# Kernel tuning notes

Hardware: AMD Instinct MI355X
Metric: run time of the kernel (lower is better)

Reference implementation:

```python
import jax, jax.numpy as jnp
import numpy as np

N = 50000          # nodes
E_RAND = 800000    # random edges
E = E_RAND + N     # + self loops -> 850000
F_IN = 256         # nembed
F_HID = 64         # nhid
H = 8              # nheads
NCLASS = 40
ALPHA = 0.2        # leakyrelu slope


def setup_inputs() -> dict:
    key = jax.random.key(0)
    ks = jax.random.split(key, 8)
    x = jax.random.normal(ks[0], (N, F_IN), dtype=jnp.float32)
    # random edges + self loops (guarantees every row-sum > 0, like adj + I)
    er = jax.random.randint(ks[1], (2, E_RAND), 0, N, dtype=jnp.int32)
    loops = jnp.tile(jnp.arange(N, dtype=jnp.int32)[None, :], (2, 1))
    edge_index = jnp.concatenate([er, loops], axis=1)  # [2, E]
    # per-head attention params (xavier-ish scale)
    W = jax.random.normal(ks[2], (H, F_IN, F_HID), dtype=jnp.float32) * (1.0 / np.sqrt(F_IN))
    a = jax.random.normal(ks[3], (H, 2 * F_HID), dtype=jnp.float32) * 0.1
    Wo = jax.random.normal(ks[4], (H * F_HID, F_HID), dtype=jnp.float32) * (1.0 / np.sqrt(H * F_HID))
    ao = jax.random.normal(ks[5], (2 * F_HID,), dtype=jnp.float32) * 0.1
    mlp_w = jax.random.normal(ks[6], (NCLASS, F_HID), dtype=jnp.float32) * 0.05
    mlp_b = jnp.zeros((NCLASS,), dtype=jnp.float32)
    return {"x": x, "edge_index": edge_index, "W": W, "a": a,
            "Wo": Wo, "ao": ao, "mlp_w": mlp_w, "mlp_b": mlp_b}


def _leaky(v):
    return jnp.where(v > 0, v, ALPHA * v)


def _spgat_layer(x, W, a, src, dst, n):
    """pyGAT SpGraphAttentionLayer (eval mode, dropout = identity).
    out[i] = sum_{e: src=i} exp(-leakyrelu(a.[h_src;h_dst])) * h[dst] / rowsum_i
    """
    h = x @ W                         # [N, D]
    D = W.shape[1]
    s_src = h @ a[:D]                 # [N]
    s_dst = h @ a[D:]                 # [N]
    # per-edge unnormalized attention (note the -exp(leaky) of original sp impl)
    e = jnp.exp(-_leaky(s_src[src] + s_dst[dst]))          # [E]
    rowsum = jax.ops.segment_sum(e, src, num_segments=n)   # [N]
    num = jax.ops.segment_sum(e[:, None] * h[dst], src, num_segments=n)  # [N, D]
    return num / rowsum[:, None]


def reference(x, edge_index, W, a, Wo, ao, mlp_w, mlp_b):
    src, dst = edge_index[0], edge_index[1]
    # multi-head attention, concat=True -> elu inside each head
    heads = [jax.nn.elu(_spgat_layer(x, W[i], a[i], src, dst, N)) for i in range(H)]
    xc = jnp.concatenate(heads, axis=1)                     # [N, H*F_HID]
    # dropout (eval) = identity
    xo = jax.nn.elu(_spgat_layer(xc, Wo, ao, src, dst, N))  # [N, F_HID]
    return xo @ mlp_w.T + mlp_b                             # [N, NCLASS]
```

## Files before the change

kernel.cpp:

```cpp
#include <hip/hip_runtime.h>

#define NN 50000
#define HH 8
#define ALPHA 0.2f
#define NPAD 50048

typedef short short8 __attribute__((ext_vector_type(8)));
typedef float f32x4 __attribute__((ext_vector_type(4)));

__device__ __forceinline__ float elu_f(float x) {
  return x > 0.f ? x : __expf(x) - 1.f;
}

__device__ __forceinline__ unsigned short f2bf(float f) {
  unsigned int u = __float_as_uint(f);
  unsigned int r = (u + 0x7fffu + ((u >> 16) & 1u)) >> 16;
  return (unsigned short)r;
}

__global__ void cvt_w_kernel(const float* __restrict__ W, unsigned short* __restrict__ Wt,
                             const float* __restrict__ Wo, unsigned short* __restrict__ Wot) {
  int tid = blockIdx.x * 256 + threadIdx.x;
  if (tid < HH * 256 * 64) {
    int h = tid / (256 * 64);
    int rem = tid - h * 256 * 64;
    int k = rem >> 6, c = rem & 63;
    Wt[((size_t)h * 64 + c) * 256 + k] = f2bf(W[tid]);
    return;
  }
  int t2 = tid - HH * 256 * 64;
  if (t2 < 512 * 64) {
    int k = t2 >> 6, c = t2 & 63;
    Wot[(size_t)c * 512 + k] = f2bf(Wo[t2]);
  }
}

__global__ void hist_kernel(const int* __restrict__ src, int* __restrict__ cnt, int E) {
  int e = blockIdx.x * blockDim.x + threadIdx.x;
  if (e < E) atomicAdd(&cnt[src[e]], 1);
}

__global__ __launch_bounds__(1024) void scan_blocks_kernel(const int* __restrict__ cnt,
    int* __restrict__ tmp, int* __restrict__ bsum, int n) {
  __shared__ int sh[1024];
  int i = blockIdx.x * 1024 + threadIdx.x;
  int v = (i < n) ? cnt[i] : 0;
  sh[threadIdx.x] = v;
  __syncthreads();
  for (int off = 1; off < 1024; off <<= 1) {
    int t = (threadIdx.x >= off) ? sh[threadIdx.x - off] : 0;
    __syncthreads();
    sh[threadIdx.x] += t;
    __syncthreads();
  }
  if (i < n) tmp[i] = sh[threadIdx.x] - v;
  if (threadIdx.x == 1023) bsum[blockIdx.x] = sh[1023];
}

__global__ __launch_bounds__(64) void scan_top_kernel(const int* __restrict__ bsum,
    int* __restrict__ boffs, int nb) {
  int L = threadIdx.x;
  int v = (L < nb) ? bsum[L] : 0;
  int incl = v;
#pragma unroll
  for (int off = 1; off < 64; off <<= 1) {
    int t = __shfl_up(incl, off, 64);
    if (L >= off) incl += t;
  }
  if (L < nb) boffs[L] = incl - v;
}

__global__ __launch_bounds__(1024) void scan_apply_kernel(const int* __restrict__ tmp,
    const int* __restrict__ boffs, int* __restrict__ row_ptr, int* __restrict__ nxt,
    int n, int E) {
  int i = blockIdx.x * 1024 + threadIdx.x;
  if (i < n) {
    int s = tmp[i] + boffs[blockIdx.x];
    row_ptr[i] = s;
    nxt[i] = s;
  }
  if (i == 0) row_ptr[n] = E;
}

__global__ void scatter_kernel(const int* __restrict__ src, const int* __restrict__ dst,
                               int* __restrict__ nxt, int* __restrict__ col, int E) {
  int e = blockIdx.x * blockDim.x + threadIdx.x;
  if (e < E) {
    int p = atomicAdd(&nxt[src[e]], 1);
    col[p] = dst[e];
  }
}

__global__ __launch_bounds__(256) void mfma_gemm1_kernel(
    const float* __restrict__ X, const unsigned short* __restrict__ Bt,
    const float* __restrict__ Aatt, unsigned short* __restrict__ Cout,
    float* __restrict__ ss, float* __restrict__ sd, int N) {
  __shared__ unsigned short Bs[64][264];
  int w = threadIdx.x >> 6, L = threadIdx.x & 63;
  int quad = L >> 4, l16 = L & 15;
  int m0 = blockIdx.x * 64;
  int myrow = m0 + w * 16 + l16;
  int rowc = min(myrow, N - 1);

  const float* Ar = X + (size_t)rowc * 256 + quad * 8;
  short8 areg[8];
#pragma unroll
  for (int ks = 0; ks < 8; ++ks) {
    float4 a0 = *(const float4*)(Ar + ks * 32);
    float4 a1 = *(const float4*)(Ar + ks * 32 + 4);
    areg[ks][0] = (short)f2bf(a0.x); areg[ks][1] = (short)f2bf(a0.y);
    areg[ks][2] = (short)f2bf(a0.z); areg[ks][3] = (short)f2bf(a0.w);
    areg[ks][4] = (short)f2bf(a1.x); areg[ks][5] = (short)f2bf(a1.y);
    areg[ks][6] = (short)f2bf(a1.z); areg[ks][7] = (short)f2bf(a1.w);
  }

  for (int y = 0; y < HH; ++y) {
    __syncthreads();
    {
      const unsigned short* Bsrc = Bt + (size_t)y * 64 * 256;
      for (int c = threadIdx.x; c < 2048; c += 256) {
        int n = c >> 5;
        int kq = (c & 31) << 3;
        *(uint4*)&Bs[n][kq] = *(const uint4*)(Bsrc + (size_t)n * 256 + kq);
      }
    }
    __syncthreads();

    f32x4 acc[4];
#pragma unroll
    for (int nt = 0; nt < 4; ++nt) acc[nt] = (f32x4)(0.f);
#pragma unroll
    for (int ks = 0; ks < 8; ++ks) {
#pragma unroll
      for (int nt = 0; nt < 4; ++nt) {
        short8 b = *(const short8*)&Bs[l16 + 16 * nt][ks * 32 + quad * 8];
        acc[nt] = __builtin_amdgcn_mfma_f32_16x16x32_bf16(areg[ks], b, acc[nt], 0, 0, 0);
      }
    }

    float as[4], ad[4];
#pragma unroll
    for (int nt = 0; nt < 4; ++nt) {
      as[nt] = Aatt[y * 128 + l16 + 16 * nt];
      ad[nt] = Aatt[y * 128 + 64 + l16 + 16 * nt];
    }
#pragma unroll
    for (int reg = 0; reg < 4; ++reg) {
      float p = 0.f, q = 0.f;
#pragma unroll
      for (int nt = 0; nt < 4; ++nt) {
        p += acc[nt][reg] * as[nt];
        q += acc[nt][reg] * ad[nt];
      }
#pragma unroll
      for (int off = 1; off < 16; off <<= 1) {
        p += __shfl_xor(p, off, 64);
        q += __shfl_xor(q, off, 64);
      }
      int row = m0 + w * 16 + quad * 4 + reg;
      if (l16 == 0 && row < N) {
        ss[(size_t)row * 8 + y] = p;
        sd[(size_t)row * 8 + y] = q;
      }
    }
#pragma unroll
    for (int reg = 0; reg < 4; ++reg) {
      int row = m0 + w * 16 + quad * 4 + reg;
      if (row < N) {
#pragma unroll
        for (int nt = 0; nt < 4; ++nt)
          Cout[(size_t)row * 512 + y * 64 + l16 + 16 * nt] = f2bf(acc[nt][reg]);
      }
    }
  }
}

__global__ __launch_bounds__(256) void mfma_gemm2_kernel(
    const unsigned short* __restrict__ A, const unsigned short* __restrict__ Bt,
    const float* __restrict__ Aatt, unsigned short* __restrict__ Cout,
    float* __restrict__ ss, float* __restrict__ sd, int N) {
  __shared__ unsigned short Bs[64][520];
  {
    for (int c = threadIdx.x; c < 4096; c += 256) {
      int n = c >> 6;
      int kq = (c & 63) << 3;
      *(uint4*)&Bs[n][kq] = *(const uint4*)(Bt + (size_t)n * 512 + kq);
    }
  }
  __syncthreads();

  int w = threadIdx.x >> 6, L = threadIdx.x & 63;
  int quad = L >> 4, l16 = L & 15;
  int m0 = blockIdx.x * 64;
  int myrow = m0 + w * 16 + l16;
  const unsigned short* Ar = A + (size_t)myrow * 512 + quad * 8;

  f32x4 acc[4];
#pragma unroll
  for (int nt = 0; nt < 4; ++nt) acc[nt] = (f32x4)(0.f);

  short8 a_cur = *(const short8*)(Ar);
  for (int k0 = 0; k0 < 512; k0 += 32) {
    short8 a_nxt;
    if (k0 + 32 < 512) a_nxt = *(const short8*)(Ar + k0 + 32);
#pragma unroll
    for (int nt = 0; nt < 4; ++nt) {
      short8 b = *(const short8*)&Bs[l16 + 16 * nt][k0 + quad * 8];
      acc[nt] = __builtin_amdgcn_mfma_f32_16x16x32_bf16(a_cur, b, acc[nt], 0, 0, 0);
    }
    a_cur = a_nxt;
  }

  float as[4], ad[4];
#pragma unroll
  for (int nt = 0; nt < 4; ++nt) {
    as[nt] = Aatt[l16 + 16 * nt];
    ad[nt] = Aatt[64 + l16 + 16 * nt];
  }
#pragma unroll
  for (int reg = 0; reg < 4; ++reg) {
    float p = 0.f, q = 0.f;
#pragma unroll
    for (int nt = 0; nt < 4; ++nt) {
      p += acc[nt][reg] * as[nt];
      q += acc[nt][reg] * ad[nt];
    }
#pragma unroll
    for (int off = 1; off < 16; off <<= 1) {
      p += __shfl_xor(p, off, 64);
      q += __shfl_xor(q, off, 64);
    }
    int row = m0 + w * 16 + quad * 4 + reg;
    if (l16 == 0 && row < N) { ss[row] = p; sd[row] = q; }
  }
#pragma unroll
  for (int reg = 0; reg < 4; ++reg) {
    int row = m0 + w * 16 + quad * 4 + reg;
    if (row < N) {
#pragma unroll
      for (int nt = 0; nt < 4; ++nt)
        Cout[(size_t)row * 64 + l16 + 16 * nt] = f2bf(acc[nt][reg]);
    }
  }
}

__global__ __launch_bounds__(256) void agg1_kernel(const unsigned short* __restrict__ table,
    const float* __restrict__ ss, const float* __restrict__ sd,
    const int* __restrict__ row_ptr, const int* __restrict__ col,
    unsigned short* __restrict__ xc, int N) {
  int bid = blockIdx.x;
  int r8 = bid & 7;
  int p = r8 >> 2;
  int nb = ((bid >> 3) << 2) | (r8 & 3);
  int wid = threadIdx.x >> 6, L = threadIdx.x & 63;
  int n = nb * 4 + wid;
  if (n >= N) return;
  int hq = L >> 4;
  int h = p * 4 + hq;
  int el = L & 15;
  float ssn = ss[n * 8 + h];
  int k0 = row_ptr[n], deg = row_ptr[n + 1] - k0;
  float acc[4] = {0.f, 0.f, 0.f, 0.f};
  float rs = 0.f;
  const char* tb = (const char*)table + p * 512;

  for (int c0 = 0; c0 < deg; c0 += 64) {
    int j = c0 + L;
    int d_l = (j < deg) ? col[k0 + j] : 0;
    int m = min(64, deg - c0);
    for (int g = 0; g < m; g += 16) {
      int eoff = g + el;
      int de = __shfl(d_l, eoff, 64);
      float s = ssn + sd[(size_t)de * 8 + h];
      float e = __expf(-fmaxf(s, ALPHA * s));
      if (eoff >= m) e = 0.f;
      rs += e;
      int gm = min(16, m - g);
      uint2 rv[16];
#pragma unroll
      for (int t = 0; t < 16; ++t) {
        if (t < gm) {
          int dg = __builtin_amdgcn_readlane(d_l, g + t);
          rv[t] = *(const uint2*)(tb + (size_t)dg * 1024 + L * 8);
        }
      }
#pragma unroll
      for (int t = 0; t < 16; ++t) {
        if (t < gm) {
          float ew = __shfl(e, (hq << 4) + t, 64);
          acc[0] += ew * __uint_as_float(rv[t].x << 16);
          acc[1] += ew * __uint_as_float(rv[t].x & 0xffff0000u);
          acc[2] += ew * __uint_as_float(rv[t].y << 16);
          acc[3] += ew * __uint_as_float(rv[t].y & 0xffff0000u);
        }
      }
    }
  }
  rs += __shfl_xor(rs, 1, 64);
  rs += __shfl_xor(rs, 2, 64);
  rs += __shfl_xor(rs, 4, 64);
  rs += __shfl_xor(rs, 8, 64);
  float inv = 1.f / rs;
  ushort4 pk;
  pk.x = f2bf(elu_f(acc[0] * inv));
  pk.y = f2bf(elu_f(acc[1] * inv));
  pk.z = f2bf(elu_f(acc[2] * inv));
  pk.w = f2bf(elu_f(acc[3] * inv));
  *(ushort4*)(xc + (size_t)n * 512 + p * 256 + L * 4) = pk;
}

__global__ __launch_bounds__(256) void agg2_final_kernel(const unsigned short* __restrict__ table,
    const float* __restrict__ ss, const float* __restrict__ sd,
    const int* __restrict__ row_ptr, const int* __restrict__ col,
    const float* __restrict__ mlp_w, const float* __restrict__ mlp_b,
    float* __restrict__ out, int N) {
  __shared__ float wsh[40 * 65];
  __shared__ float bsh[40];
  __shared__ float osh[4][68];
  for (int i = threadIdx.x; i < 40 * 64; i += 256) wsh[(i >> 6) * 65 + (i & 63)] = mlp_w[i];
  if (threadIdx.x < 40) bsh[threadIdx.x] = mlp_b[threadIdx.x];
  __syncthreads();

  int wid = threadIdx.x >> 6, L = threadIdx.x & 63;
  int n = blockIdx.x * 4 + wid;
  bool act = (n < N);
  float o = 0.f;
  if (act) {
    float ssn = ss[n];
    int k0 = row_ptr[n], deg = row_ptr[n + 1] - k0;
    float acc = 0.f, rs = 0.f;
    const char* base = (const char*)table;
    for (int c0 = 0; c0 < deg; c0 += 64) {
      int j = c0 + L;
      int d_l = 0;
      float e_l = 0.f;
      if (j < deg) {
        d_l = col[k0 + j];
        float s = ssn + sd[d_l];
        e_l = __expf(-fmaxf(s, ALPHA * s));
      }
      rs += e_l;
      int m = min(64, deg - c0);
      int off_l = d_l << 7;
      for (int g = 0; g < m; g += 8) {
        int gm = min(8, m - g);
        unsigned hv[8];
#pragma unroll
        for (int t = 0; t < 8; ++t) {
          if (t < gm) {
            int so = __builtin_amdgcn_readlane(off_l, g + t);
            hv[t] = *(const unsigned short*)(base + so + L * 2);
          }
        }
#pragma unroll
        for (int t = 0; t < 8; ++t) {
          if (t < gm) {
            float ew = __uint_as_float(
                (unsigned)__builtin_amdgcn_readlane(__float_as_uint(e_l), g + t));
            acc += ew * __uint_as_float(hv[t] << 16);
          }
        }
      }
    }
#pragma unroll
    for (int off = 1; off < 64; off <<= 1) rs += __shfl_xor(rs, off, 64);
    o = elu_f(acc / rs);
  }
  osh[wid][L] = o;
  __syncthreads();
  if (act && L < 40) {
    const float* wr = wsh + L * 65;
    const float* orow = osh[wid];
    float acc = bsh[L];
#pragma unroll
    for (int j = 0; j < 64; ++j) acc += orow[j] * wr[j];
    out[(size_t)n * 40 + L] = acc;
  }
}

extern "C" void kernel_launch(void* const* d_in, const int* in_sizes, int n_in,
                              void* d_out, int out_size, void* d_ws, size_t ws_size,
                              hipStream_t stream) {
  (void)n_in; (void)out_size; (void)ws_size;
  const float* x  = (const float*)d_in[0];
  const int*   ei = (const int*)d_in[1];
  const float* W  = (const float*)d_in[2];
  const float* a  = (const float*)d_in[3];
  const float* Wo = (const float*)d_in[4];
  const float* ao = (const float*)d_in[5];
  const float* mw = (const float*)d_in[6];
  const float* mb = (const float*)d_in[7];
  float* out = (float*)d_out;

  const int N = NN;
  const int E = in_sizes[1] / 2;
  const int* src = ei;
  const int* dst = ei + E;

  char* ws = (char*)d_ws;
  size_t off = 0;
  auto alloc = [&](size_t bytes) {
    char* p = ws + off;
    off = (off + bytes + 255) & ~(size_t)255;
    return p;
  };
  unsigned short* Wt  = (unsigned short*)alloc((size_t)HH * 64 * 256 * 2);
  unsigned short* Wot = (unsigned short*)alloc((size_t)64 * 512 * 2);
  unsigned short* h1b = (unsigned short*)alloc((size_t)N * 512 * 2);
  float* ss1     = (float*)alloc((size_t)N * 8 * 4);
  float* sd1     = (float*)alloc((size_t)N * 8 * 4);
  unsigned short* xc = (unsigned short*)alloc((size_t)NPAD * 512 * 2);
  unsigned short* h2b = (unsigned short*)alloc((size_t)N * 64 * 2);
  float* ss2     = (float*)alloc((size_t)N * 4);
  float* sd2     = (float*)alloc((size_t)N * 4);
  int*   row_ptr = (int*)  alloc((size_t)(N + 1) * 4);
  int*   nxt     = (int*)  alloc((size_t)N * 4);
  int*   cnt     = (int*)  alloc((size_t)N * 4);
  int*   tmp     = (int*)  alloc((size_t)N * 4);
  int*   bsum    = (int*)  alloc(64 * 4);
  int*   boffs   = (int*)  alloc(64 * 4);
  int*   colv    = (int*)  alloc((size_t)E * 4);

  int eb = (E + 255) / 256;
  int nb1024 = (N + 1023) / 1024;

  hipLaunchKernelGGL(cvt_w_kernel, dim3((HH * 256 * 64 + 512 * 64 + 255) / 256), dim3(256),
                     0, stream, W, Wt, Wo, Wot);

  hipMemsetAsync(cnt, 0, (size_t)N * 4, stream);
  hipLaunchKernelGGL(hist_kernel, dim3(eb), dim3(256), 0, stream, src, cnt, E);
  hipLaunchKernelGGL(scan_blocks_kernel, dim3(nb1024), dim3(1024), 0, stream, cnt, tmp, bsum, N);
  hipLaunchKernelGGL(scan_top_kernel, dim3(1), dim3(64), 0, stream, bsum, boffs, nb1024);
  hipLaunchKernelGGL(scan_apply_kernel, dim3(nb1024), dim3(1024), 0, stream, tmp, boffs, row_ptr, nxt, N, E);
  hipLaunchKernelGGL(scatter_kernel, dim3(eb), dim3(256), 0, stream, src, dst, nxt, colv, E);

  hipLaunchKernelGGL(mfma_gemm1_kernel, dim3(NPAD / 64), dim3(256), 0, stream,
                     x, Wt, a, h1b, ss1, sd1, N);
  hipLaunchKernelGGL(agg1_kernel, dim3(2 * ((N + 3) / 4)), dim3(256), 0, stream,
                     h1b, ss1, sd1, row_ptr, colv, xc, N);

  hipLaunchKernelGGL(mfma_gemm2_kernel, dim3(NPAD / 64), dim3(256), 0, stream,
                     xc, Wot, ao, h2b, ss2, sd2, N);
  hipLaunchKernelGGL(agg2_final_kernel, dim3((N + 3) / 4), dim3(256), 0, stream,
                     h2b, ss2, sd2, row_ptr, colv, mw, mb, out, N);
}
```

Measured before the change: 441.4 us.

## Store layer-1 features head-major and aggregate one head per block slice

```diff
diff --git a/kernel.cpp b/kernel.cpp
--- a/kernel.cpp
+++ b/kernel.cpp
@@ -57,25 +57,21 @@
   if (threadIdx.x == 1023) bsum[blockIdx.x] = sh[1023];
 }
 
-__global__ __launch_bounds__(64) void scan_top_kernel(const int* __restrict__ bsum,
-    int* __restrict__ boffs, int nb) {
-  int L = threadIdx.x;
-  int v = (L < nb) ? bsum[L] : 0;
-  int incl = v;
-#pragma unroll
-  for (int off = 1; off < 64; off <<= 1) {
-    int t = __shfl_up(incl, off, 64);
-    if (L >= off) incl += t;
-  }
-  if (L < nb) boffs[L] = incl - v;
-}
-
 __global__ __launch_bounds__(1024) void scan_apply_kernel(const int* __restrict__ tmp,
-    const int* __restrict__ boffs, int* __restrict__ row_ptr, int* __restrict__ nxt,
-    int n, int E) {
+    const int* __restrict__ bsum, int* __restrict__ row_ptr, int* __restrict__ nxt,
+    int n, int E, int nb) {
+  __shared__ int boff_sh;
+  if (threadIdx.x < 64) {
+    int L = threadIdx.x;
+    int v = (L < nb && L < (int)blockIdx.x) ? bsum[L] : 0;
+#pragma unroll
+    for (int off = 1; off < 64; off <<= 1) v += __shfl_xor(v, off, 64);
+    if (L == 0) boff_sh = v;
+  }
+  __syncthreads();
   int i = blockIdx.x * 1024 + threadIdx.x;
   if (i < n) {
-    int s = tmp[i] + boffs[blockIdx.x];
+    int s = tmp[i] + boff_sh;
     row_ptr[i] = s;
     nxt[i] = s;
   }
@@ -169,7 +165,7 @@
       if (row < N) {
 #pragma unroll
         for (int nt = 0; nt < 4; ++nt)
-          Cout[(size_t)row * 512 + y * 64 + l16 + 16 * nt] = f2bf(acc[nt][reg]);
+          Cout[((size_t)y * N + row) * 64 + l16 + 16 * nt] = f2bf(acc[nt][reg]);
       }
     }
   }
@@ -248,65 +244,53 @@
     const float* __restrict__ ss, const float* __restrict__ sd,
     const int* __restrict__ row_ptr, const int* __restrict__ col,
     unsigned short* __restrict__ xc, int N) {
-  int bid = blockIdx.x;
-  int r8 = bid & 7;
-  int p = r8 >> 2;
-  int nb = ((bid >> 3) << 2) | (r8 & 3);
+  int h = blockIdx.y;
   int wid = threadIdx.x >> 6, L = threadIdx.x & 63;
-  int n = nb * 4 + wid;
+  int n = blockIdx.x * 4 + wid;
   if (n >= N) return;
-  int hq = L >> 4;
-  int h = p * 4 + hq;
-  int el = L & 15;
   float ssn = ss[n * 8 + h];
   int k0 = row_ptr[n], deg = row_ptr[n + 1] - k0;
-  float acc[4] = {0.f, 0.f, 0.f, 0.f};
-  float rs = 0.f;
-  const char* tb = (const char*)table + p * 512;
+  const unsigned short* tab = table + (size_t)h * N * 64;
+  int half = L >> 5;
+  int fd = L & 31;
+  float a0 = 0.f, a1 = 0.f, rs = 0.f;
 
   for (int c0 = 0; c0 < deg; c0 += 64) {
     int j = c0 + L;
-    int d_l = (j < deg) ? col[k0 + j] : 0;
+    int d_l = 0;
+    float e_l = 0.f;
+    if (j < deg) {
+      d_l = col[k0 + j];
+      float s = ssn + sd[(size_t)d_l * 8 + h];
+      e_l = __expf(-fmaxf(s, ALPHA * s));
+    }
+    rs += e_l;
     int m = min(64, deg - c0);
     for (int g = 0; g < m; g += 16) {
-      int eoff = g + el;
-      int de = __shfl(d_l, eoff, 64);
-      float s = ssn + sd[(size_t)de * 8 + h];
-      float e = __expf(-fmaxf(s, ALPHA * s));
-      if (eoff >= m) e = 0.f;
-      rs += e;
-      int gm = min(16, m - g);
-      uint2 rv[16];
-#pragma unroll
-      for (int t = 0; t < 16; ++t) {
-        if (t < gm) {
-          int dg = __builtin_amdgcn_readlane(d_l, g + t);
-          rv[t] = *(const uint2*)(tb + (size_t)dg * 1024 + L * 8);
-        }
-      }
-#pragma unroll
-      for (int t = 0; t < 16; ++t) {
-        if (t < gm) {
-          float ew = __shfl(e, (hq << 4) + t, 64);
-          acc[0] += ew * __uint_as_float(rv[t].x << 16);
-          acc[1] += ew * __uint_as_float(rv[t].x & 0xffff0000u);
-          acc[2] += ew * __uint_as_float(rv[t].y << 16);
-          acc[3] += ew * __uint_as_float(rv[t].y & 0xffff0000u);
-        }
-      }
-    }
-  }
-  rs += __shfl_xor(rs, 1, 64);
-  rs += __shfl_xor(rs, 2, 64);
-  rs += __shfl_xor(rs, 4, 64);
-  rs += __shfl_xor(rs, 8, 64);
-  float inv = 1.f / rs;
-  ushort4 pk;
-  pk.x = f2bf(elu_f(acc[0] * inv));
-  pk.y = f2bf(elu_f(acc[1] * inv));
-  pk.z = f2bf(elu_f(acc[2] * inv));
-  pk.w = f2bf(elu_f(acc[3] * inv));
-  *(ushort4*)(xc + (size_t)n * 512 + p * 256 + L * 4) = pk;
+      unsigned rv[8];
+#pragma unroll
+      for (int t = 0; t < 8; ++t) {
+        int dg = __shfl(d_l, g + 2 * t + half, 64);
+        rv[t] = *(const unsigned*)(tab + (size_t)dg * 64 + fd * 2);
+      }
+#pragma unroll
+      for (int t = 0; t < 8; ++t) {
+        float ew = __shfl(e_l, g + 2 * t + half, 64);
+        a0 += ew * __uint_as_float(rv[t] << 16);
+        a1 += ew * __uint_as_float(rv[t] & 0xffff0000u);
+      }
+    }
+  }
+  a0 += __shfl_xor(a0, 32, 64);
+  a1 += __shfl_xor(a1, 32, 64);
+#pragma unroll
+  for (int off = 1; off < 64; off <<= 1) rs += __shfl_xor(rs, off, 64);
+  if (L < 32) {
+    float inv = 1.f / rs;
+    unsigned p0 = f2bf(elu_f(a0 * inv));
+    unsigned p1 = f2bf(elu_f(a1 * inv));
+    *(unsigned*)(xc + (size_t)n * 512 + h * 64 + fd * 2) = p0 | (p1 << 16);
+  }
 }
 
 __global__ __launch_bounds__(256) void agg2_final_kernel(const unsigned short* __restrict__ table,
@@ -406,7 +390,7 @@
   };
   unsigned short* Wt  = (unsigned short*)alloc((size_t)HH * 64 * 256 * 2);
   unsigned short* Wot = (unsigned short*)alloc((size_t)64 * 512 * 2);
-  unsigned short* h1b = (unsigned short*)alloc((size_t)N * 512 * 2);
+  unsigned short* h1b = (unsigned short*)alloc((size_t)HH * N * 64 * 2);
   float* ss1     = (float*)alloc((size_t)N * 8 * 4);
   float* sd1     = (float*)alloc((size_t)N * 8 * 4);
   unsigned short* xc = (unsigned short*)alloc((size_t)NPAD * 512 * 2);
@@ -418,7 +402,6 @@
   int*   cnt     = (int*)  alloc((size_t)N * 4);
   int*   tmp     = (int*)  alloc((size_t)N * 4);
   int*   bsum    = (int*)  alloc(64 * 4);
-  int*   boffs   = (int*)  alloc(64 * 4);
   int*   colv    = (int*)  alloc((size_t)E * 4);
 
   int eb = (E + 255) / 256;
@@ -430,13 +413,13 @@
   hipMemsetAsync(cnt, 0, (size_t)N * 4, stream);
   hipLaunchKernelGGL(hist_kernel, dim3(eb), dim3(256), 0, stream, src, cnt, E);
   hipLaunchKernelGGL(scan_blocks_kernel, dim3(nb1024), dim3(1024), 0, stream, cnt, tmp, bsum, N);
-  hipLaunchKernelGGL(scan_top_kernel, dim3(1), dim3(64), 0, stream, bsum, boffs, nb1024);
-  hipLaunchKernelGGL(scan_apply_kernel, dim3(nb1024), dim3(1024), 0, stream, tmp, boffs, row_ptr, nxt, N, E);
+  hipLaunchKernelGGL(scan_apply_kernel, dim3(nb1024), dim3(1024), 0, stream,
+                     tmp, bsum, row_ptr, nxt, N, E, nb1024);
   hipLaunchKernelGGL(scatter_kernel, dim3(eb), dim3(256), 0, stream, src, dst, nxt, colv, E);
 
   hipLaunchKernelGGL(mfma_gemm1_kernel, dim3(NPAD / 64), dim3(256), 0, stream,
                      x, Wt, a, h1b, ss1, sd1, N);
-  hipLaunchKernelGGL(agg1_kernel, dim3(2 * ((N + 3) / 4)), dim3(256), 0, stream,
+  hipLaunchKernelGGL(agg1_kernel, dim3((N + 3) / 4, HH), dim3(256), 0, stream,
                      h1b, ss1, sd1, row_ptr, colv, xc, N);
 
   hipLaunchKernelGGL(mfma_gemm2_kernel, dim3(NPAD / 64), dim3(256), 0, stream,
```

After: 471.3 us. +6.8%, slower.
